# Kernel tuning notes

Measured on AMD Instinct MI355X. Metric: run time of the kernel, lower is better.

Reference implementation:

```python
import jax, jax.numpy as jnp
import numpy as np
import math

B, S, L, D, H, HID = 8, 512, 6, 512, 8, 2048
N_CITIES, C = 10000, 256
IN_DIM = C + 1  # pretrained out_channels + normalized demand


def setup_inputs() -> dict:
    key = jax.random.key(0)
    ks = jax.random.split(key, 32)
    # solutions: [B,S,4]; col0 = city index (int-valued float), col2 = demand, col3 = capacity state
    idx = jax.random.randint(ks[0], (B, S), 0, N_CITIES).astype(jnp.float32)
    demand = jax.random.uniform(ks[1], (B, S), minval=0.0, maxval=10.0)
    cap_state = jax.random.uniform(ks[2], (B, S), minval=20.0, maxval=100.0)
    solutions = jnp.stack([idx, jnp.zeros((B, S)), demand, cap_state], axis=-1).astype(jnp.float32)
    capacities = jax.random.uniform(ks[3], (B,), minval=50.0, maxval=100.0)

    def lin(k, fi, fo):
        kw, kb = jax.random.split(k)
        return (jax.random.normal(kw, (fi, fo)) / np.float32(math.sqrt(fi)),
                jax.random.normal(kb, (fo,)) * 0.01)

    embeddings = jax.random.normal(ks[4], (N_CITIES, C)) * 0.1
    src_W, src_b = lin(ks[5], IN_DIM, D)
    cand_W, cand_b = lin(ks[6], IN_DIM, D)
    dep_W, dep_b = lin(ks[7], IN_DIM, D)
    feas_W, feas_b = lin(ks[8], D, 1)

    def stack(kk, fi, fo):
        Ws, bs = zip(*[lin(jax.random.fold_in(kk, i), fi, fo) for i in range(L)])
        return jnp.stack(Ws), jnp.stack(bs)

    Wq, bq = stack(ks[9], D, D)
    Wk, bk = stack(ks[10], D, D)
    Wv, bv = stack(ks[11], D, D)
    Wo, bo = stack(ks[12], D, D)
    s_scale = jnp.full((L,), 0.43, dtype=jnp.float32)
    W1, b1 = stack(ks[13], D, HID)
    W2, b2 = stack(ks[14], HID, D)
    ptr_W, ptr_b = lin(ks[15], D, 2)
    return dict(solutions=solutions, capacities=capacities, embeddings=embeddings,
                src_W=src_W, src_b=src_b, cand_W=cand_W, cand_b=cand_b,
                dep_W=dep_W, dep_b=dep_b, feas_W=feas_W, feas_b=feas_b,
                Wq=Wq, bq=bq, Wk=Wk, bk=bk, Wv=Wv, bv=bv, Wo=Wo, bo=bo,
                s_scale=s_scale, W1=W1, b1=b1, W2=W2, b2=b2,
                ptr_W=ptr_W, ptr_b=ptr_b)


def _mha(x, Wq, bq, Wk, bk, Wv, bv, Wo, bo, s):
    b, n, d = x.shape
    hd = d // H
    q = (x @ Wq + bq).reshape(b, n, H, hd)
    k = (x @ Wk + bk).reshape(b, n, H, hd)
    v = (x @ Wv + bv).reshape(b, n, H, hd)
    scores = jnp.einsum('bqhd,bkhd->bhqk', q, k) / np.float32(math.sqrt(hd))
    # ScalableSoftmax: softmax(scores + s * log(n)) over last dim
    w = jax.nn.softmax(scores + s * np.float32(math.log(n)), axis=-1)
    out = jnp.einsum('bhqk,bkhd->bqhd', w, v).reshape(b, n, d)
    return out @ Wo + bo


def _forward(solutions, capacities, embeddings, src_W, src_b, cand_W, cand_b,
             dep_W, dep_b, feas_W, feas_b, Wq, bq, Wk, bk, Wv, bv, Wo, bo,
             s_scale, W1, b1, W2, b2, ptr_W, ptr_b):
    idx = jax.lax.stop_gradient(solutions)[:, :, 0].astype(jnp.int32)  # city indices
    enc = embeddings[idx]                                              # [B,S,C]
    rem = solutions[:, 0, 3]
    nd = 2.0 * ((solutions[:, :, 2] - rem[:, None]) / capacities[:, None])
    xin = jnp.concatenate([enc, nd[..., None]], axis=-1)               # [B,S,C+1]
    xin = xin.at[:, 0, -1].set(0.0)

    # NodeEmbedder: source / candidates / depot with separate linears
    src = xin[:, :1] @ src_W + src_b
    cand = xin[:, 1:-1] @ cand_W + cand_b
    dep = xin[:, -1:] @ dep_W + dep_b
    x = jnp.concatenate([src, cand, dep], axis=1)                      # [B,S,D]

    x = x + _mha(x, Wq[0], bq[0], Wk[0], bk[0], Wv[0], bv[0], Wo[0], bo[0], s_scale[0])
    feas = (x[:, 1:-1] @ feas_W + feas_b)[..., 0]                      # [B,S-2]

    for i in range(L):
        if i > 0:
            x = x + _mha(x, Wq[i], bq[i], Wk[i], bk[i], Wv[i], bv[i], Wo[i], bo[i], s_scale[i])
        x = x + (jax.nn.relu(x @ W1[i] + b1[i]) @ W2[i] + b2[i])

    logits = x @ ptr_W + ptr_b                                         # [B,S,2]
    out = jnp.concatenate([logits[:, 1:-1, 0], logits[:, 1:-1, 1]], axis=1)  # [B,2*(S-2)]
    return out, feas


def reference(solutions, capacities, embeddings, src_W, src_b, cand_W, cand_b,
              dep_W, dep_b, feas_W, feas_b, Wq, bq, Wk, bk, Wv, bv, Wo, bo,
              s_scale, W1, b1, W2, b2, ptr_W, ptr_b):
    return _forward(solutions, capacities, embeddings, src_W, src_b, cand_W, cand_b,
                    dep_W, dep_b, feas_W, feas_b, Wq, bq, Wk, bk, Wv, bv, Wo, bo,
                    s_scale, W1, b1, W2, b2, ptr_W, ptr_b)
```

## Files before the change

kernel.cpp:

```cpp
#include <hip/hip_runtime.h>

typedef unsigned short u16;
typedef _Float16 half8 __attribute__((ext_vector_type(8)));
typedef float f32x4 __attribute__((ext_vector_type(4)));

__device__ inline float bf2f(u16 b) { return __builtin_bit_cast(float, ((unsigned)b) << 16); }
__device__ inline float h2f(u16 h) { return (float)__builtin_bit_cast(_Float16, h); }
__device__ inline u16 f2h_bits(float f) { return __builtin_bit_cast(u16, (_Float16)f); }

__device__ inline int detect_bf16(const void* caps) {
    const u16* c = (const u16*)caps;
    int cnt = 0;
#pragma unroll
    for (int k = 0; k < 4; ++k) {
        float v = bf2f(c[2 * k]);
        if (v >= 20.f && v <= 200.f) cnt++;
    }
    return cnt >= 2;
}
__device__ inline float ldin(const void* p, size_t i, int flag) {
    return flag ? bf2f(((const u16*)p)[i]) : ((const float*)p)[i];
}

#define GLOAD_LDS16(g, l)                                                              \
    __builtin_amdgcn_global_load_lds((__attribute__((address_space(1))) const void*)(g), \
                                     (__attribute__((address_space(3))) void*)(l), 16, 0, 0)

template <int N>
__device__ inline void waitv() {
    if constexpr (N == 0)      asm volatile("s_waitcnt vmcnt(0)" ::: "memory");
    else if constexpr (N == 3) asm volatile("s_waitcnt vmcnt(3)" ::: "memory");
    else if constexpr (N == 4) asm volatile("s_waitcnt vmcnt(4)" ::: "memory");
    else if constexpr (N == 6) asm volatile("s_waitcnt vmcnt(6)" ::: "memory");
    else if constexpr (N == 8) asm volatile("s_waitcnt vmcnt(8)" ::: "memory");
}
__device__ inline void barrier_raw() {
    asm volatile("" ::: "memory");
    __builtin_amdgcn_s_barrier();
    asm volatile("" ::: "memory");
}

#define A_SRCW 0
#define A_SRCB 131584
#define A_CANDW 132096
#define A_CANDB 263680
#define A_DEPW 264192
#define A_DEPB 395776
#define A_FEASW 396288
#define A_FEASB 396800
#define A_PW 396801
#define A_PB 397825
#define A_BO 397827
#define A_B1 400899
#define A_B2 413187
#define A_TOTAL 416259

template <int CF, int BN>
__global__ __launch_bounds__(256) void gemm_f16(
    const u16* __restrict__ A, int lda,
    const u16* __restrict__ B, int ldb,
    void* __restrict__ Cv, int ldc,
    const float* __restrict__ bias, float* __restrict__ resid,
    u16* __restrict__ vtp,
    float scale, int relu, int N, int K)
{
    constexpr int NT = BN / 32;
    constexpr int S = (BN == 128) ? 4 : 3;
    __shared__ __attribute__((aligned(16))) u16 As[4][128 * 32];
    __shared__ __attribute__((aligned(16))) u16 Bs[4][BN * 32];

    const int gx = gridDim.x, gy = gridDim.y;
    int mb, nb;
    if ((gy & 7) == 0) {
        int id = blockIdx.x + blockIdx.y * gx;
        int xcd = id & 7, local = id >> 3;
        int mloc = local / gx;
        mb = xcd * (gy >> 3) + mloc;
        nb = local - mloc * gx;
    } else {
        mb = blockIdx.y;
        nb = blockIdx.x;
    }
    const int m0 = mb * 128;
    const int n0 = nb * BN;

    const int t = threadIdx.x, lane = t & 63, wid = t >> 6;
    const int qd = lane >> 4, ml = lane & 15;
    const int wm = (wid >> 1) * 64, wn = (wid & 1) * (BN / 2);

    f32x4 acc[4][NT] = {};

    auto stage = [&](int bf, int k0) {
#pragma unroll
        for (int rep = 0; rep < 2; ++rep) {
            int seg = (wid + rep * 4) * 64 + lane;
            int row = seg >> 2, c8 = (seg & 3) * 8;
            const u16* ga = A + (long long)(m0 + row) * lda + k0 + c8;
            GLOAD_LDS16(ga, As[bf] + (size_t)(seg & ~63) * 8);
            if (BN == 128 || rep == 0) {
                int rn = n0 + row;
                if (rn > N - 1) rn = N - 1;
                const u16* gb = B + (long long)rn * ldb + k0 + c8;
                GLOAD_LDS16(gb, Bs[bf] + (size_t)(seg & ~63) * 8);
            }
        }
    };

    auto compute = [&](int bf) {
        half8 af[4], bfv[NT];
#pragma unroll
        for (int mt = 0; mt < 4; ++mt)
            af[mt] = *(const half8*)(As[bf] + (wm + mt * 16 + ml) * 32 + qd * 8);
#pragma unroll
        for (int nt = 0; nt < NT; ++nt)
            bfv[nt] = *(const half8*)(Bs[bf] + (wn + nt * 16 + ml) * 32 + qd * 8);
#pragma unroll
        for (int mt = 0; mt < 4; ++mt)
#pragma unroll
            for (int nt = 0; nt < NT; ++nt)
                acc[mt][nt] = __builtin_amdgcn_mfma_f32_16x16x32_f16(af[mt], bfv[nt], acc[mt][nt], 0, 0, 0);
    };

    stage(0, 0);
    if (K > 32) stage(1, 32);

    int buf = 0, k0 = 0;
    for (; k0 + 64 < K; k0 += 32) {
        stage((buf + 2) & 3, k0 + 64);
        waitv<2 * S>();
        barrier_raw();
        compute(buf);
        buf = (buf + 1) & 3;
    }
    if (k0 + 32 < K) {
        waitv<S>();
        barrier_raw();
        compute(buf);
        buf = (buf + 1) & 3;
        k0 += 32;
    }
    waitv<0>();
    barrier_raw();
    compute(buf);

#pragma unroll
    for (int nt = 0; nt < NT; ++nt) {
        int col = n0 + wn + nt * 16 + ml;
        if (col >= N) continue;
        float bv = bias ? bias[col] : 0.f;
#pragma unroll
        for (int mt = 0; mt < 4; ++mt) {
#pragma unroll
            for (int r = 0; r < 4; ++r) {
                int rowg = m0 + wm + mt * 16 + qd * 4 + r;
                float v = acc[mt][nt][r] * scale + bv;
                if (relu) v = fmaxf(v, 0.f);
                long long off = (long long)rowg * ldc + col;
                if (CF == 1) {
                    ((float*)Cv)[off] = v;
                } else if (CF == 2) {
                    resid[off] = v;
                    ((u16*)Cv)[off] = f2h_bits(v);
                } else if (resid) {
                    float nv = resid[off] + v;
                    resid[off] = nv;
                    ((u16*)Cv)[off] = f2h_bits(nv);
                } else if (vtp && col >= 1024) {
                    int b = rowg >> 9, s = rowg & 511;
                    int cv2 = col - 1024;
                    vtp[(size_t)(((b << 3) + (cv2 >> 6)) * 32768 + (cv2 & 63) * 512 + s)] = f2h_bits(v);
                } else {
                    ((u16*)Cv)[off] = f2h_bits(v);
                }
            }
        }
    }
}

__global__ __launch_bounds__(256) void flash_k(
    const u16* __restrict__ qkv,
    const u16* __restrict__ vt,
    u16* __restrict__ ob)
{
    __shared__ __attribute__((aligned(16))) u16 Ps[128 * 136];

    int id = blockIdx.x + (blockIdx.y << 2);
    int xcd = id & 7, local = id >> 3;
    const int z = (xcd << 3) + (local >> 2);
    const int q0 = (local & 3) * 128;

    const int b = z >> 3, h = z & 7;
    const long long qbase = (long long)b * 786432;
    const u16* Q  = qkv + qbase + (long long)q0 * 1536 + h * 64;
    const u16* Kg = qkv + qbase + 512 + h * 64;
    const u16* Vg = vt + (long long)z * 32768;

    const int t = threadIdx.x, lane = t & 63, wid = t >> 6;
    const int qd = lane >> 4, ml = lane & 15;
    const int wm = wid * 32;

    half8 qf[2][2];
#pragma unroll
    for (int mt = 0; mt < 2; ++mt)
#pragma unroll
        for (int kf = 0; kf < 2; ++kf)
            qf[mt][kf] = *(const half8*)(Q + (long long)(wm + mt * 16 + ml) * 1536 + kf * 32 + qd * 8);

    f32x4 oacc[2][4] = {};
    float mrow[2][4], lrow[2][4];
#pragma unroll
    for (int mt = 0; mt < 2; ++mt)
#pragma unroll
        for (int r = 0; r < 4; ++r) { mrow[mt][r] = -3.0e38f; lrow[mt][r] = 0.f; }

    for (int kb = 0; kb < 4; ++kb) {
        f32x4 sacc[2][8] = {};
#pragma unroll
        for (int nt = 0; nt < 8; ++nt) {
#pragma unroll
            for (int kf = 0; kf < 2; ++kf) {
                half8 bf = *(const half8*)(Kg + (long long)(kb * 128 + nt * 16 + ml) * 1536 + kf * 32 + qd * 8);
#pragma unroll
                for (int mt = 0; mt < 2; ++mt)
                    sacc[mt][nt] = __builtin_amdgcn_mfma_f32_16x16x32_f16(qf[mt][kf], bf, sacc[mt][nt], 0, 0, 0);
            }
        }
#pragma unroll
        for (int mt = 0; mt < 2; ++mt) {
#pragma unroll
            for (int r = 0; r < 4; ++r) {
                float mx = -3.0e38f;
#pragma unroll
                for (int nt = 0; nt < 8; ++nt) {
                    float s = sacc[mt][nt][r] * 0.125f;
                    sacc[mt][nt][r] = s;
                    mx = fmaxf(mx, s);
                }
#pragma unroll
                for (int o = 1; o < 16; o <<= 1) mx = fmaxf(mx, __shfl_xor(mx, o, 64));
                float mnew = fmaxf(mrow[mt][r], mx);
                float alpha = __expf(mrow[mt][r] - mnew);
                mrow[mt][r] = mnew;
                lrow[mt][r] *= alpha;
#pragma unroll
                for (int nt = 0; nt < 4; ++nt) oacc[mt][nt][r] *= alpha;
                float ps = 0.f;
#pragma unroll
                for (int nt = 0; nt < 8; ++nt) {
                    float p = __expf(sacc[mt][nt][r] - mnew);
                    sacc[mt][nt][r] = p;
                    ps += p;
                }
#pragma unroll
                for (int o = 1; o < 16; o <<= 1) ps += __shfl_xor(ps, o, 64);
                lrow[mt][r] += ps;
            }
        }
#pragma unroll
        for (int mt = 0; mt < 2; ++mt)
#pragma unroll
            for (int nt = 0; nt < 8; ++nt)
#pragma unroll
                for (int r = 0; r < 4; ++r)
                    Ps[(wm + mt * 16 + qd * 4 + r) * 136 + nt * 16 + ml] = f2h_bits(sacc[mt][nt][r]);
#pragma unroll
        for (int kf = 0; kf < 4; ++kf) {
            half8 pf[2];
#pragma unroll
            for (int mt = 0; mt < 2; ++mt)
                pf[mt] = *(const half8*)(Ps + (wm + mt * 16 + ml) * 136 + kf * 32 + qd * 8);
#pragma unroll
            for (int nt = 0; nt < 4; ++nt) {
                half8 vf = *(const half8*)(Vg + (long long)(nt * 16 + ml) * 512 + kb * 128 + kf * 32 + qd * 8);
#pragma unroll
                for (int mt = 0; mt < 2; ++mt)
                    oacc[mt][nt] = __builtin_amdgcn_mfma_f32_16x16x32_f16(pf[mt], vf, oacc[mt][nt], 0, 0, 0);
            }
        }
    }

#pragma unroll
    for (int mt = 0; mt < 2; ++mt) {
#pragma unroll
        for (int r = 0; r < 4; ++r) {
            float inv = 1.f / lrow[mt][r];
            long long rowg = (long long)b * 512 + q0 + wm + mt * 16 + qd * 4 + r;
#pragma unroll
            for (int nt = 0; nt < 4; ++nt)
                ob[rowg * 512 + h * 64 + nt * 16 + ml] = f2h_bits(oacc[mt][nt][r] * inv);
        }
    }
}

template <int MODE>
__global__ void transpose_k(const void* __restrict__ src_, int s_ld, long long s_off,
                            long long s_so, long long s_si,
                            u16* __restrict__ dst, int d_ld, long long d_so, long long d_si,
                            int R, int Rs, int C, const void* caps)
{
    __shared__ u16 tile[32][33];
    const int z = blockIdx.z;
    const long long sb = s_off + (long long)(z >> 3) * s_so + (long long)(z & 7) * s_si;
    dst += (long long)(z >> 3) * d_so + (long long)(z & 7) * d_si;
    const int c0 = blockIdx.x * 32, r0 = blockIdx.y * 32;
    const int tx = threadIdx.x, ty = threadIdx.y;
    const int flag = (MODE == 1) ? detect_bf16(caps) : 0;
#pragma unroll
    for (int i = 0; i < 4; ++i) {
        int r = r0 + ty + i * 8, c = c0 + tx;
        if (r < R && c < C) {
            u16 v = 0;
            if (r < Rs) {
                size_t idx = (size_t)(sb + (long long)r * s_ld + c);
                if (MODE == 1) v = f2h_bits(ldin(src_, idx, flag));
                else           v = ((const u16*)src_)[idx];
            }
            tile[ty + i * 8][tx] = v;
        }
    }
    __syncthreads();
#pragma unroll
    for (int i = 0; i < 4; ++i) {
        int r = r0 + tx, c = c0 + ty + i * 8;
        if (r < R && c < C) dst[(long long)c * d_ld + r] = tile[tx][ty + i * 8];
    }
}

__global__ void qkvoT6_k(const void* Wq, const void* Wk, const void* Wv, const void* Wo,
                         u16* __restrict__ wqkvT6, u16* __restrict__ woT6,
                         const void* caps)
{
    __shared__ u16 tile[32][33];
    const int z = blockIdx.z;
    const int layer = z >> 2, sel = z & 3;
    const void* src = (sel == 0) ? Wq : (sel == 1) ? Wk : (sel == 2) ? Wv : Wo;
    u16* dst = (sel < 3) ? (wqkvT6 + (long long)layer * 786432 + (long long)sel * 262144)
                         : (woT6 + (long long)layer * 262144);
    const long long oW = (long long)layer * 262144;
    const int c0 = blockIdx.x * 32, r0 = blockIdx.y * 32;
    const int tx = threadIdx.x, ty = threadIdx.y;
    const int flag = detect_bf16(caps);
#pragma unroll
    for (int i = 0; i < 4; ++i) {
        int r = r0 + ty + i * 8, c = c0 + tx;
        tile[ty + i * 8][tx] = f2h_bits(ldin(src, (size_t)(oW + (long long)r * 512 + c), flag));
    }
    __syncthreads();
#pragma unroll
    for (int i = 0; i < 4; ++i) {
        int r = r0 + tx, c = c0 + ty + i * 8;
        dst[(long long)c * 512 + r] = tile[tx][ty + i * 8];
    }
}

__global__ void cvt_small_k(const void* srcW, const void* srcB, const void* candW, const void* candB,
                            const void* depW, const void* depB, const void* feasW, const void* feasB,
                            const void* pW, const void* pb, const void* boi, const void* b1i,
                            const void* b2i, const void* caps, float* __restrict__ dst)
{
    int i = blockIdx.x * 256 + threadIdx.x;
    if (i >= A_TOTAL) return;
    int flag = detect_bf16(caps);
    const void* s; int j;
    if      (i < A_SRCB)  { s = srcW;  j = i - A_SRCW; }
    else if (i < A_CANDW) { s = srcB;  j = i - A_SRCB; }
    else if (i < A_CANDB) { s = candW; j = i - A_CANDW; }
    else if (i < A_DEPW)  { s = candB; j = i - A_CANDB; }
    else if (i < A_DEPB)  { s = depW;  j = i - A_DEPW; }
    else if (i < A_FEASW) { s = depB;  j = i - A_DEPB; }
    else if (i < A_FEASB) { s = feasW; j = i - A_FEASW; }
    else if (i < A_PW)    { s = feasB; j = i - A_FEASB; }
    else if (i < A_PB)    { s = pW;    j = i - A_PW; }
    else if (i < A_BO)    { s = pb;    j = i - A_PB; }
    else if (i < A_B1)    { s = boi;   j = i - A_BO; }
    else if (i < A_B2)    { s = b1i;   j = i - A_B1; }
    else                  { s = b2i;   j = i - A_B2; }
    dst[i] = ldin(s, j, flag);
}

__global__ void catbias_k(const void* bq, const void* bk, const void* bv,
                          const void* caps, float* __restrict__ dst)
{
    int t = blockIdx.x * 256 + threadIdx.x;
    if (t >= 6 * 1536) return;
    int flag = detect_bf16(caps);
    int l = t / 1536, j = t - l * 1536;
    float v = (j < 512) ? ldin(bq, l * 512 + j, flag)
            : (j < 1024) ? ldin(bk, l * 512 + j - 512, flag)
                         : ldin(bv, l * 512 + j - 1024, flag);
    dst[t] = v;
}

__global__ __launch_bounds__(256) void gather_xin_k(
    const void* __restrict__ sol, const void* __restrict__ caps, const void* __restrict__ emb,
    u16* __restrict__ xin)
{
    const int row = blockIdx.x;
    const int b = row >> 9, s = row & 511;
    const int t = threadIdx.x;
    const int flag = detect_bf16(caps);
    float idxf = ldin(sol, (size_t)row * 4, flag);
    int idx = (int)(idxf + 0.5f);
    if (idx < 0) idx = 0;
    if (idx > 9999) idx = 9999;
    xin[(size_t)row * 288 + t] = f2h_bits(ldin(emb, (size_t)idx * 256 + t, flag));
    if (t < 32) {
        float v = 0.f;
        if (t == 0 && s != 0) {
            float rem = ldin(sol, ((size_t)b * 512) * 4 + 3, flag);
            float cap = ldin(caps, b, flag);
            float dem = ldin(sol, (size_t)row * 4 + 2, flag);
            v = 2.f * (dem - rem) / cap;
        }
        xin[(size_t)row * 288 + 256 + t] = f2h_bits(v);
    }
}

__global__ __launch_bounds__(256) void fixup_enc_k(
    const void* __restrict__ sol, const void* __restrict__ caps, const void* __restrict__ emb,
    const float* __restrict__ arena, float* __restrict__ xf, u16* __restrict__ xb)
{
    const int blk = blockIdx.x;
    const int b = blk & 7;
    const int s = (blk >> 3) ? 511 : 0;
    const int row = b * 512 + s;
    const int t = threadIdx.x;
    __shared__ float e[256];
    __shared__ float nds;
    const int flag = detect_bf16(caps);
    float idxf = ldin(sol, (size_t)row * 4, flag);
    int idx = (int)(idxf + 0.5f);
    if (idx < 0) idx = 0;
    if (idx > 9999) idx = 9999;
    e[t] = ldin(emb, (size_t)idx * 256 + t, flag);
    if (t == 0) {
        float rem = ldin(sol, ((size_t)b * 512) * 4 + 3, flag);
        float cap = ldin(caps, b, flag);
        float dem = ldin(sol, (size_t)row * 4 + 2, flag);
        nds = (s == 0) ? 0.f : 2.f * (dem - rem) / cap;
    }
    __syncthreads();
    const float* W  = (s == 0) ? arena + A_SRCW : arena + A_DEPW;
    const float* Bb = (s == 0) ? arena + A_SRCB : arena + A_DEPB;
    float a0 = 0.f, a1 = 0.f;
    for (int c = 0; c < 256; ++c) {
        float ev = e[c];
        a0 += ev * W[(size_t)c * 512 + t];
        a1 += ev * W[(size_t)c * 512 + t + 256];
    }
    float nd = nds;
    a0 += nd * W[256 * 512 + t] + Bb[t];
    a1 += nd * W[256 * 512 + t + 256] + Bb[t + 256];
    size_t o = (size_t)row * 512;
    xf[o + t] = a0;        xb[o + t] = f2h_bits(a0);
    xf[o + t + 256] = a1;  xb[o + t + 256] = f2h_bits(a1);
}

__global__ __launch_bounds__(256) void feas_k(const float* __restrict__ xf,
                                              const float* __restrict__ arena,
                                              float* __restrict__ out)
{
    int w = blockIdx.x * 4 + (threadIdx.x >> 6);
    if (w >= 8 * 510) return;
    int lane = threadIdx.x & 63;
    int b = w / 510, j = w - b * 510;
    const float* xr = xf + ((size_t)(b * 512 + 1 + j)) * 512;
    const float* fW = arena + A_FEASW;
    float a = 0.f;
#pragma unroll
    for (int i = 0; i < 8; ++i) { int d = lane + 64 * i; a += xr[d] * fW[d]; }
#pragma unroll
    for (int o = 1; o < 64; o <<= 1) a += __shfl_xor(a, o, 64);
    if (lane == 0) out[8160 + b * 510 + j] = a + arena[A_FEASB];
}

__global__ __launch_bounds__(256) void ptr_k(const float* __restrict__ xf,
                                             const float* __restrict__ arena,
                                             float* __restrict__ out)
{
    int w = blockIdx.x * 4 + (threadIdx.x >> 6);
    if (w >= 8 * 510) return;
    int lane = threadIdx.x & 63;
    int b = w / 510, j = w - b * 510;
    const float* xr = xf + ((size_t)(b * 512 + 1 + j)) * 512;
    const float* pWa = arena + A_PW;
    float a0 = 0.f, a1 = 0.f;
#pragma unroll
    for (int i = 0; i < 8; ++i) {
        int d = lane + 64 * i;
        float x = xr[d];
        a0 += x * pWa[d * 2];
        a1 += x * pWa[d * 2 + 1];
    }
#pragma unroll
    for (int o = 1; o < 64; o <<= 1) { a0 += __shfl_xor(a0, o, 64); a1 += __shfl_xor(a1, o, 64); }
    if (lane == 0) {
        out[(size_t)b * 1020 + j]       = a0 + arena[A_PB];
        out[(size_t)b * 1020 + 510 + j] = a1 + arena[A_PB + 1];
    }
}

extern "C" void kernel_launch(void* const* d_in, const int* in_sizes, int n_in,
                              void* d_out, int out_size, void* d_ws, size_t ws_size,
                              hipStream_t stream)
{
    const void* sol   = d_in[0];
    const void* caps  = d_in[1];
    const void* emb   = d_in[2];
    const void* srcW  = d_in[3];
    const void* srcB  = d_in[4];
    const void* candW = d_in[5];
    const void* candB = d_in[6];
    const void* depW  = d_in[7];
    const void* depB  = d_in[8];
    const void* feasW = d_in[9];
    const void* feasB = d_in[10];
    const void* Wq  = d_in[11];
    const void* bq  = d_in[12];
    const void* Wk  = d_in[13];
    const void* bk  = d_in[14];
    const void* Wv  = d_in[15];
    const void* bv  = d_in[16];
    const void* Wo  = d_in[17];
    const void* boi = d_in[18];
    const void* W1  = d_in[20];
    const void* b1i = d_in[21];
    const void* W2  = d_in[22];
    const void* b2i = d_in[23];
    const void* pW  = d_in[24];
    const void* pb  = d_in[25];
    float* out = (float*)d_out;

    char* w = (char*)d_ws;
    float* xf    = (float*)w; w += 8388608;
    u16* xb      = (u16*)w;   w += 4194304;
    u16* qkvb    = (u16*)w;   w += 12582912;
    u16* vt      = (u16*)w;   w += 4194304;
    u16* hb      = (u16*)w;   w += 16777216;
    u16* xin     = hb;
    u16* encW    = hb + 4096 * 288;
    u16* ob      = (u16*)w;   w += 4194304;
    u16* wqkvT6  = (u16*)w;   w += 9437184;
    u16* woT6    = (u16*)w;   w += 3145728;
    u16* w1T6    = (u16*)w;   w += 12582912;
    u16* w2T6    = (u16*)w;   w += 12582912;
    float* bqkvf = (float*)w; w += 36864;
    float* arena = (float*)w; w += A_TOTAL * 4;

    dim3 tb(32, 8);
    cvt_small_k<<<dim3((A_TOTAL + 255) / 256), 256, 0, stream>>>(
        srcW, srcB, candW, candB, depW, depB, feasW, feasB, pW, pb, boi, b1i, b2i, caps, arena);
    catbias_k<<<dim3(36), 256, 0, stream>>>(bq, bk, bv, caps, bqkvf);

    qkvoT6_k<<<dim3(16, 16, 24), tb, 0, stream>>>(Wq, Wk, Wv, Wo, wqkvT6, woT6, caps);
    transpose_k<1><<<dim3(64, 16, 6), tb, 0, stream>>>(W1, 2048, 0, 0, 1048576,
                                                       w1T6, 512, 0, 1048576, 512, 512, 2048, caps);
    transpose_k<1><<<dim3(16, 64, 6), tb, 0, stream>>>(W2, 512, 0, 0, 1048576,
                                                       w2T6, 2048, 0, 1048576, 2048, 2048, 512, caps);

    gather_xin_k<<<dim3(4096), 256, 0, stream>>>(sol, caps, emb, xin);
    transpose_k<1><<<dim3(16, 9, 1), tb, 0, stream>>>(candW, 512, 0, 0, 0,
                                                      encW, 288, 0, 0, 288, 257, 512, caps);
    gemm_f16<2, 64><<<dim3(8, 32), 256, 0, stream>>>(
        xin, 288, encW, 288,
        xb, 512, arena + A_CANDB, xf, nullptr, 1.f, 0, 512, 288);
    fixup_enc_k<<<dim3(16), 256, 0, stream>>>(sol, caps, emb, arena, xf, xb);

    for (int i = 0; i < 6; ++i) {
        gemm_f16<0, 64><<<dim3(24, 32), 256, 0, stream>>>(
            xb, 512, wqkvT6 + (long long)i * 786432, 512,
            qkvb, 1536, bqkvf + i * 1536, nullptr, vt, 1.f, 0, 1536, 512);

        flash_k<<<dim3(4, 64), 256, 0, stream>>>(qkvb, vt, ob);

        gemm_f16<0, 64><<<dim3(8, 32), 256, 0, stream>>>(
            ob, 512, woT6 + (long long)i * 262144, 512,
            xb, 512, arena + A_BO + i * 512, xf, nullptr, 1.f, 0, 512, 512);
        if (i == 0)
            feas_k<<<dim3(1020), 256, 0, stream>>>(xf, arena, out);

        gemm_f16<0, 128><<<dim3(16, 32), 256, 0, stream>>>(
            xb, 512, w1T6 + (long long)i * 1048576, 512,
            hb, 2048, arena + A_B1 + i * 2048, nullptr, nullptr, 1.f, 1, 2048, 512);

        gemm_f16<0, 64><<<dim3(8, 32), 256, 0, stream>>>(
            hb, 2048, w2T6 + (long long)i * 1048576, 2048,
            xb, 512, arena + A_B2 + i * 512, xf, nullptr, 1.f, 0, 512, 2048);
    }
    ptr_k<<<dim3(1020), 256, 0, stream>>>(xf, arena, out);
}
```

Measured before the change: 942.9 us.

## Halve GEMM M-tile, add XOR-swizzled LDS layout, and raise MFMA priority in flash

Makes the GEMM M tile a template parameter and launches every GEMM with 64-row tiles, doubling the grid so more workgroups cover the 256 CUs. The global-to-LDS staging and the fragment reads now use an XOR swizzle on the 16-byte column chunk to cut LDS bank conflicts. The flash attention kernel also raises wave priority around its MFMA blocks. Smaller tiles lower per-block reuse and raise total global traffic, in exchange for better occupancy and load balance.

```diff
diff --git a/kernel.cpp b/kernel.cpp
--- a/kernel.cpp
+++ b/kernel.cpp
@@ -29,6 +29,7 @@
 template <int N>
 __device__ inline void waitv() {
     if constexpr (N == 0)      asm volatile("s_waitcnt vmcnt(0)" ::: "memory");
+    else if constexpr (N == 2) asm volatile("s_waitcnt vmcnt(2)" ::: "memory");
     else if constexpr (N == 3) asm volatile("s_waitcnt vmcnt(3)" ::: "memory");
     else if constexpr (N == 4) asm volatile("s_waitcnt vmcnt(4)" ::: "memory");
     else if constexpr (N == 6) asm volatile("s_waitcnt vmcnt(6)" ::: "memory");
@@ -55,7 +56,7 @@
 #define A_B2 413187
 #define A_TOTAL 416259
 
-template <int CF, int BN>
+template <int CF, int BM, int BN>
 __global__ __launch_bounds__(256) void gemm_f16(
     const u16* __restrict__ A, int lda,
     const u16* __restrict__ B, int ldb,
@@ -64,9 +65,10 @@
     u16* __restrict__ vtp,
     float scale, int relu, int N, int K)
 {
+    constexpr int MT = BM / 32;
     constexpr int NT = BN / 32;
-    constexpr int S = (BN == 128) ? 4 : 3;
-    __shared__ __attribute__((aligned(16))) u16 As[4][128 * 32];
+    constexpr int S = BM / 64 + BN / 64;
+    __shared__ __attribute__((aligned(16))) u16 As[4][BM * 32];
     __shared__ __attribute__((aligned(16))) u16 Bs[4][BN * 32];
 
     const int gx = gridDim.x, gy = gridDim.y;
@@ -81,41 +83,47 @@
         mb = blockIdx.y;
         nb = blockIdx.x;
     }
-    const int m0 = mb * 128;
+    const int m0 = mb * BM;
     const int n0 = nb * BN;
 
     const int t = threadIdx.x, lane = t & 63, wid = t >> 6;
     const int qd = lane >> 4, ml = lane & 15;
-    const int wm = (wid >> 1) * 64, wn = (wid & 1) * (BN / 2);
-
-    f32x4 acc[4][NT] = {};
+    const int wm = (wid >> 1) * (BM / 2), wn = (wid & 1) * (BN / 2);
+    const int cs = (qd ^ (ml & 3)) * 8;
+
+    f32x4 acc[MT][NT] = {};
 
     auto stage = [&](int bf, int k0) {
 #pragma unroll
-        for (int rep = 0; rep < 2; ++rep) {
-            int seg = (wid + rep * 4) * 64 + lane;
-            int row = seg >> 2, c8 = (seg & 3) * 8;
+        for (int r = 0; r < BM / 64; ++r) {
+            int seg = r * 256 + t;
+            int row = seg >> 2;
+            int c8 = (((seg & 3) ^ (row & 3)) * 8);
             const u16* ga = A + (long long)(m0 + row) * lda + k0 + c8;
             GLOAD_LDS16(ga, As[bf] + (size_t)(seg & ~63) * 8);
-            if (BN == 128 || rep == 0) {
-                int rn = n0 + row;
-                if (rn > N - 1) rn = N - 1;
-                const u16* gb = B + (long long)rn * ldb + k0 + c8;
-                GLOAD_LDS16(gb, Bs[bf] + (size_t)(seg & ~63) * 8);
-            }
+        }
+#pragma unroll
+        for (int r = 0; r < BN / 64; ++r) {
+            int seg = r * 256 + t;
+            int row = seg >> 2;
+            int c8 = (((seg & 3) ^ (row & 3)) * 8);
+            int rn = n0 + row;
+            if (rn > N - 1) rn = N - 1;
+            const u16* gb = B + (long long)rn * ldb + k0 + c8;
+            GLOAD_LDS16(gb, Bs[bf] + (size_t)(seg & ~63) * 8);
         }
     };
 
     auto compute = [&](int bf) {
-        half8 af[4], bfv[NT];
-#pragma unroll
-        for (int mt = 0; mt < 4; ++mt)
-            af[mt] = *(const half8*)(As[bf] + (wm + mt * 16 + ml) * 32 + qd * 8);
+        half8 af[MT], bfv[NT];
+#pragma unroll
+        for (int mt = 0; mt < MT; ++mt)
+            af[mt] = *(const half8*)(As[bf] + (wm + mt * 16 + ml) * 32 + cs);
 #pragma unroll
         for (int nt = 0; nt < NT; ++nt)
-            bfv[nt] = *(const half8*)(Bs[bf] + (wn + nt * 16 + ml) * 32 + qd * 8);
-#pragma unroll
-        for (int mt = 0; mt < 4; ++mt)
+            bfv[nt] = *(const half8*)(Bs[bf] + (wn + nt * 16 + ml) * 32 + cs);
+#pragma unroll
+        for (int mt = 0; mt < MT; ++mt)
 #pragma unroll
             for (int nt = 0; nt < NT; ++nt)
                 acc[mt][nt] = __builtin_amdgcn_mfma_f32_16x16x32_f16(af[mt], bfv[nt], acc[mt][nt], 0, 0, 0);
@@ -149,7 +157,7 @@
         if (col >= N) continue;
         float bv = bias ? bias[col] : 0.f;
 #pragma unroll
-        for (int mt = 0; mt < 4; ++mt) {
+        for (int mt = 0; mt < MT; ++mt) {
 #pragma unroll
             for (int r = 0; r < 4; ++r) {
                 int rowg = m0 + wm + mt * 16 + qd * 4 + r;
@@ -215,6 +223,7 @@
 
     for (int kb = 0; kb < 4; ++kb) {
         f32x4 sacc[2][8] = {};
+        __builtin_amdgcn_s_setprio(1);
 #pragma unroll
         for (int nt = 0; nt < 8; ++nt) {
 #pragma unroll
@@ -225,6 +234,7 @@
                     sacc[mt][nt] = __builtin_amdgcn_mfma_f32_16x16x32_f16(qf[mt][kf], bf, sacc[mt][nt], 0, 0, 0);
             }
         }
+        __builtin_amdgcn_s_setprio(0);
 #pragma unroll
         for (int mt = 0; mt < 2; ++mt) {
 #pragma unroll
@@ -263,6 +273,7 @@
 #pragma unroll
                 for (int r = 0; r < 4; ++r)
                     Ps[(wm + mt * 16 + qd * 4 + r) * 136 + nt * 16 + ml] = f2h_bits(sacc[mt][nt][r]);
+        __builtin_amdgcn_s_setprio(1);
 #pragma unroll
         for (int kf = 0; kf < 4; ++kf) {
             half8 pf[2];
@@ -277,6 +288,7 @@
                     oacc[mt][nt] = __builtin_amdgcn_mfma_f32_16x16x32_f16(pf[mt], vf, oacc[mt][nt], 0, 0, 0);
             }
         }
+        __builtin_amdgcn_s_setprio(0);
     }
 
 #pragma unroll
@@ -561,29 +573,29 @@
     gather_xin_k<<<dim3(4096), 256, 0, stream>>>(sol, caps, emb, xin);
     transpose_k<1><<<dim3(16, 9, 1), tb, 0, stream>>>(candW, 512, 0, 0, 0,
                                                       encW, 288, 0, 0, 288, 257, 512, caps);
-    gemm_f16<2, 64><<<dim3(8, 32), 256, 0, stream>>>(
+    gemm_f16<2, 64, 64><<<dim3(8, 64), 256, 0, stream>>>(
         xin, 288, encW, 288,
         xb, 512, arena + A_CANDB, xf, nullptr, 1.f, 0, 512, 288);
     fixup_enc_k<<<dim3(16), 256, 0, stream>>>(sol, caps, emb, arena, xf, xb);
 
     for (int i = 0; i < 6; ++i) {
-        gemm_f16<0, 64><<<dim3(24, 32), 256, 0, stream>>>(
+        gemm_f16<0, 64, 64><<<dim3(24, 64), 256, 0, stream>>>(
             xb, 512, wqkvT6 + (long long)i * 786432, 512,
             qkvb, 1536, bqkvf + i * 1536, nullptr, vt, 1.f, 0, 1536, 512);
 
         flash_k<<<dim3(4, 64), 256, 0, stream>>>(qkvb, vt, ob);
 
-        gemm_f16<0, 64><<<dim3(8, 32), 256, 0, stream>>>(
+        gemm_f16<0, 64, 64><<<dim3(8, 64), 256, 0, stream>>>(
             ob, 512, woT6 + (long long)i * 262144, 512,
             xb, 512, arena + A_BO + i * 512, xf, nullptr, 1.f, 0, 512, 512);
         if (i == 0)
             feas_k<<<dim3(1020), 256, 0, stream>>>(xf, arena, out);
 
-        gemm_f16<0, 128><<<dim3(16, 32), 256, 0, stream>>>(
+        gemm_f16<0, 64, 128><<<dim3(16, 64), 256, 0, stream>>>(
             xb, 512, w1T6 + (long long)i * 1048576, 512,
             hb, 2048, arena + A_B1 + i * 2048, nullptr, nullptr, 1.f, 1, 2048, 512);
 
-        gemm_f16<0, 64><<<dim3(8, 32), 256, 0, stream>>>(
+        gemm_f16<0, 64, 64><<<dim3(8, 64), 256, 0, stream>>>(
             hb, 2048, w2T6 + (long long)i * 1048576, 2048,
             xb, 512, arena + A_B2 + i * 512, xf, nullptr, 1.f, 0, 512, 2048);
     }
```

New measurement: 955.2 us. Within noise of the previous version (+1.3%).
